# Performance work log

Hardware: AMD Instinct MI355X
Metric: run time of the kernel (lower is better)

## Reference

```python
import jax, jax.numpy as jnp
import numpy as np

B, L, D = 8, 2048, 1024


def _hippo(d, seed=0):
    # Author's 'hippo_matrix': Q @ diag(arctan(linspace(0, pi, d))) @ Q.T with Q orthogonal.
    rng = np.random.default_rng(seed)
    Q, _ = np.linalg.qr(rng.standard_normal((d, d)))
    Dm = np.diag(np.arctan(np.linspace(0.0, np.pi, d)))
    return (Q @ Dm @ Q.T).astype(np.float32)


def setup_inputs() -> dict:
    key = jax.random.key(0)
    k1, k2, k3, k4 = jax.random.split(key, 4)
    x = jax.random.normal(k1, (B, L, D), jnp.float32)
    A_w = jnp.asarray(_hippo(D))                                   # [D, D], spectral norm <= arctan(pi)
    C_w = jax.random.normal(k2, (D, D), jnp.float32) * (D ** -0.5)  # readout C
    # rc maps cat(x_t, y_{t-1}, y_container) (3D) -> D; small init keeps the
    # linear recurrence spectral radius < 1 so the 2048-step scan stays finite.
    rc_w = jax.random.normal(k3, (D, 3 * D), jnp.float32) * (0.2 / np.sqrt(3 * D))
    rc_b = jax.random.normal(k4, (D,), jnp.float32) * 0.02
    return {"x": x, "A_w": A_w, "C_w": C_w, "rc_w": rc_w, "rc_b": rc_b}


def reference(x, A_w, C_w, rc_w, rc_b):
    # y[0] = x[0]; y[t] = C @ A @ (rc_w @ cat(x[t], y[t-1], y[t-1]) + rc_b)
    # (prev output enters twice: once via the outer forward_step cat, once via
    #  the LinearRecurrentContainer's internal memory y).
    d = x.shape[-1]
    Wx = rc_w[:, :d]                          # acts on x_t
    Wy = rc_w[:, d:2 * d] + rc_w[:, 2 * d:]   # both copies of y_{t-1}
    M = C_w @ A_w                             # fused C∘A readout, [D, D]
    P = M @ Wx                                # input map
    Q = M @ Wy                                # recurrence map
    c = M @ rc_b                              # fused bias
    u = jnp.einsum('bld,ed->ble', x[:, 1:], P) + c  # driving terms for t >= 1, [B, L-1, D]
    y0 = x[:, 0]                              # parallel_scan copies the first input verbatim

    def step(y_prev, u_t):
        y = u_t + y_prev @ Q.T                # [B, D]
        return y, y

    _, ys = jax.lax.scan(step, y0, jnp.swapaxes(u, 0, 1))  # [L-1, B, D]
    return jnp.concatenate([y0[:, None, :], jnp.swapaxes(ys, 0, 1)], axis=1)  # [B, L, D]
```

## Files before the change

### kernel.cpp

```cpp
#include <hip/hip_runtime.h>

typedef unsigned short u16;
typedef unsigned int   u32;
typedef __attribute__((ext_vector_type(8))) short short8;
typedef __attribute__((ext_vector_type(4))) short short4v;
typedef __attribute__((ext_vector_type(4))) float f32x4;

struct SqJobs {
  const u16* a[4];
  const u16* b[4];
  u16* c[4];
  u16* ct[4];
};

__device__ __forceinline__ float bf2f(u16 v) {
  u32 x = ((u32)v) << 16;
  return __builtin_bit_cast(float, x);
}
__device__ __forceinline__ u16 f2bf(float f) {
  u32 x = __builtin_bit_cast(u32, f);
  x += 0x7FFFu + ((x >> 16) & 1u);
  return (u16)(x >> 16);
}
__device__ __forceinline__ void gload_lds16(const u16* g, u16* l) {
  __builtin_amdgcn_global_load_lds(
      (const __attribute__((address_space(1))) u32*)g,
      (__attribute__((address_space(3))) u32*)l, 16, 0, 0);
}

template <int BM, int BN, int ADT, int BDT, int EPI, int AMAP, int OMAP,
          int COUT, int TRW, int SQF>
__global__ __launch_bounds__(256) void gemm_nt(
    const void* __restrict__ Av, int lda, const void* __restrict__ Bv, int ldb,
    void* __restrict__ Cv, int ldc, int Mrows, int K,
    const float* __restrict__ zrowF, const u16* __restrict__ zrowB,
    const float* __restrict__ bias, const float* __restrict__ addf,
    float* __restrict__ Yout, u16* __restrict__ aux16, int jp1, int shoff,
    SqJobs jb) {
  constexpr int WM = BM / 2, WN = BN / 2;
  constexpr int MT = WM / 16, NTT = WN / 16;
  constexpr int AIn = ADT ? BM * 8 : BM * 4;
  constexpr int BIn = BDT ? BN * 8 : BN * 4;
  static_assert(AIn >= 256 && BIn >= 256, "tile too small for 256 threads");
  constexpr int AI = AIn / 256, BI = BIn / 256;
  constexpr int LA = BM * 32, LB = BN * 32;
  __shared__ u16 lA[2 * LA];
  __shared__ u16 lB[2 * LB];
  const int tid = threadIdx.x;
  const int lane = tid & 63, wid = tid >> 6;
  const int wm = wid & 1, wn = wid >> 1;
  const bool role = (SQF == 1) && ((int)blockIdx.x >= 32);
  const int pi = role ? (((int)blockIdx.x - 32) >> 4) : 0;
  const int bxe = role ? (((int)blockIdx.x - 32) & 15) : (int)blockIdx.x;
  const int m0 = bxe * BM, n0 = blockIdx.y * BN;
  const int effM = role ? 1024 : Mrows;
  const int q = lane >> 4, lm = lane & 15;
  const int cq = (q ^ (lm & 3)) * 8;

  const u16* corrB = nullptr;
  if constexpr (EPI == 7)
    corrB = (blockIdx.z == 0)
                ? (const u16*)Bv
                : jb.a[0] + (long)((int)blockIdx.z - 1) * 1048576;

  f32x4 acc[MT][NTT];
#pragma unroll
  for (int mi = 0; mi < MT; ++mi)
#pragma unroll
    for (int ni = 0; ni < NTT; ++ni) acc[mi][ni] = (f32x4){0.f, 0.f, 0.f, 0.f};

  const u16* aB[AI];
  const float* aF[AI];
#pragma unroll
  for (int i = 0; i < AI; ++i) {
    int g = tid + i * 256;
    int r = ADT ? (g >> 3) : (g >> 2);
    int c = ADT ? (g & 7) : (g & 3);
    int row = m0 + r;
    bool valid = (row < effM);
    if (AMAP == 1 && !role) {
      int p = row % 257;
      if (p < shoff) valid = false;
      row -= shoff;
    }
    if constexpr (ADT == 1) {
      int cs = ((((c >> 1) ^ (r & 3)) << 1) | (c & 1)) * 4;
      aF[i] = (valid ? (const float*)Av + (long)row * lda : zrowF) + cs;
    } else {
      int cs = (c ^ (r & 3)) * 8;
      const u16* base;
      if (role)
        base = jb.a[pi] + (long)row * 1024;
      else
        base = valid ? (const u16*)Av + (long)row * lda : zrowB;
      aB[i] = base + cs;
    }
  }
  const u16* bB[BI];
  const float* bF[BI];
#pragma unroll
  for (int i = 0; i < BI; ++i) {
    int g = tid + i * 256;
    int r = BDT ? (g >> 3) : (g >> 2);
    int c = BDT ? (g & 7) : (g & 3);
    if constexpr (BDT == 1) {
      int cs = ((((c >> 1) ^ (r & 3)) << 1) | (c & 1)) * 4;
      bF[i] = (const float*)Bv + (long)(n0 + r) * ldb + cs;
    } else {
      int cs = (c ^ (r & 3)) * 8;
      const u16* base;
      if (role) {
        base = jb.b[pi] + (long)(n0 + r) * 1024;
      } else {
        if constexpr (EPI == 7)
          base = corrB + (long)(n0 + r) * ldb;
        else
          base = (const u16*)Bv + (long)(n0 + r) * ldb;
      }
      bB[i] = base + cs;
    }
  }

  if constexpr (ADT == 1) {
    f32x4 f0[AI];
#pragma unroll
    for (int i = 0; i < AI; ++i) f0[i] = *(const f32x4*)(aF[i]);
#pragma unroll
    for (int i = 0; i < AI; ++i) {
      short4v s = {(short)f2bf(f0[i][0]), (short)f2bf(f0[i][1]),
                   (short)f2bf(f0[i][2]), (short)f2bf(f0[i][3])};
      *(short4v*)&lA[(tid + i * 256) * 4] = s;
    }
  } else {
#pragma unroll
    for (int i = 0; i < AI; ++i) gload_lds16(aB[i], &lA[(tid + i * 256) * 8]);
  }
  if constexpr (BDT == 1) {
    f32x4 f0[BI];
#pragma unroll
    for (int i = 0; i < BI; ++i) f0[i] = *(const f32x4*)(bF[i]);
#pragma unroll
    for (int i = 0; i < BI; ++i) {
      short4v s = {(short)f2bf(f0[i][0]), (short)f2bf(f0[i][1]),
                   (short)f2bf(f0[i][2]), (short)f2bf(f0[i][3])};
      *(short4v*)&lB[(tid + i * 256) * 4] = s;
    }
  } else {
#pragma unroll
    for (int i = 0; i < BI; ++i) gload_lds16(bB[i], &lB[(tid + i * 256) * 8]);
  }
  __syncthreads();

  int cur = 0;
  for (int k0 = 0; k0 < K; k0 += 32) {
    const int kn = k0 + 32;
    const bool more = kn < K;
    const int nxA = (cur ^ 1) * LA, nxB = (cur ^ 1) * LB;
    f32x4 fa[AI], fb[BI];
    if (more) {
      if constexpr (ADT == 1) {
#pragma unroll
        for (int i = 0; i < AI; ++i) fa[i] = *(const f32x4*)(aF[i] + kn);
      } else {
#pragma unroll
        for (int i = 0; i < AI; ++i)
          gload_lds16(aB[i] + kn, &lA[nxA + (tid + i * 256) * 8]);
      }
      if constexpr (BDT == 1) {
#pragma unroll
        for (int i = 0; i < BI; ++i) fb[i] = *(const f32x4*)(bF[i] + kn);
      } else {
#pragma unroll
        for (int i = 0; i < BI; ++i)
          gload_lds16(bB[i] + kn, &lB[nxB + (tid + i * 256) * 8]);
      }
    }
    short8 af[MT], bf[NTT];
#pragma unroll
    for (int mi = 0; mi < MT; ++mi)
      af[mi] =
          *(const short8*)&lA[cur * LA + (wm * WM + mi * 16 + lm) * 32 + cq];
#pragma unroll
    for (int ni = 0; ni < NTT; ++ni)
      bf[ni] =
          *(const short8*)&lB[cur * LB + (wn * WN + ni * 16 + lm) * 32 + cq];
#pragma unroll
    for (int mi = 0; mi < MT; ++mi)
#pragma unroll
      for (int ni = 0; ni < NTT; ++ni)
        acc[mi][ni] = __builtin_amdgcn_mfma_f32_16x16x32_bf16(
            af[mi], bf[ni], acc[mi][ni], 0, 0, 0);
    if (more) {
      if constexpr (ADT == 1) {
#pragma unroll
        for (int i = 0; i < AI; ++i) {
          short4v s = {(short)f2bf(fa[i][0]), (short)f2bf(fa[i][1]),
                       (short)f2bf(fa[i][2]), (short)f2bf(fa[i][3])};
          *(short4v*)&lA[nxA + (tid + i * 256) * 4] = s;
        }
      }
      if constexpr (BDT == 1) {
#pragma unroll
        for (int i = 0; i < BI; ++i) {
          short4v s = {(short)f2bf(fb[i][0]), (short)f2bf(fb[i][1]),
                       (short)f2bf(fb[i][2]), (short)f2bf(fb[i][3])};
          *(short4v*)&lB[nxB + (tid + i * 256) * 4] = s;
        }
      }
    }
    __syncthreads();
    cur ^= 1;
  }

#pragma unroll
  for (int mi = 0; mi < MT; ++mi) {
    int rbase = m0 + wm * WM + mi * 16 + q * 4;
#pragma unroll
    for (int ni = 0; ni < NTT; ++ni) {
      int ocol = n0 + wn * WN + ni * 16 + lm;
#pragma unroll
      for (int r = 0; r < 4; ++r) {
        int orow = rbase + r;
        float v = acc[mi][ni][r];
        if (role) {
          if (orow < 1024) {
            u16 ov = f2bf(v);
            jb.c[pi][(long)orow * 1024 + ocol] = ov;
            if (jb.ct[pi]) jb.ct[pi][(long)ocol * 1024 + orow] = ov;
          }
          continue;
        }
        if (orow >= Mrows) continue;
        if constexpr (EPI == 7) {
          long urow = 8L * orow + ((int)blockIdx.z + 1);
          float vv = v + addf[urow * 1024 + ocol];
          Yout[urow * 1024 + ocol] = vv;
          continue;
        }
        if constexpr (EPI == 5) {
          v += bias[ocol];
          bool isT0 = (orow & 2047) == 0;
          if (isT0) v = addf[(long)orow * 1024 + ocol];
          ((float*)Cv)[(long)orow * ldc + ocol] = v;
          if (isT0) Yout[((long)(orow >> 11) * 257) * 1024 + ocol] = v;
          if ((orow & 7) == 1)
            aux16[((long)(orow >> 3)) * 1024 + ocol] = f2bf(v);
          continue;
        }
        if constexpr (EPI == 6) {
          v += addf[(long)orow * 1024 + ocol];
          ((float*)Cv)[(long)orow * ldc + ocol] = v;
          int b = orow / 257;
          int pp_ = orow - b * 257;
          if (pp_ < 256)
            aux16[((long)(b * 256 + pp_)) * 1024 + ocol] = f2bf(v);
          if (pp_ >= 1 && pp_ < 256)
            Yout[((long)b * 2048 + 8L * pp_) * 1024 + ocol] = v;
          continue;
        }
        long urow = 0;
        bool uok = true;
        if constexpr (EPI == 2 || EPI == 3) {
          urow = 8L * orow + jp1;
          uok = ((urow & 2047) != 0);
          if (uok) v += addf[urow * 1024 + ocol];
        }
        if constexpr (EPI == 4) v += addf[(long)orow * 1024 + ocol];
        long wrow = orow;
        if constexpr (OMAP == 1)
          wrow = (long)(orow >> 8) * 257 + (orow & 255) + 1;
        if constexpr (COUT == 1)
          ((float*)Cv)[wrow * (long)ldc + ocol] = v;
        else
          ((u16*)Cv)[wrow * (long)ldc + ocol] = f2bf(v);
        if constexpr (TRW == 1) aux16[(long)ocol * ldc + orow] = f2bf(v);
        if constexpr (EPI == 3) {
          if (uok) Yout[urow * 1024 + ocol] = v;
        }
      }
    }
  }
}

__global__ void zero_misc(float* zF, u16* zB) {
  for (int i = threadIdx.x; i < 2048; i += 256) {
    zF[i] = 0.f;
    zB[i] = 0;
  }
}
__global__ void xconv(const float* __restrict__ x, u16* __restrict__ xb) {
  long i = (long)blockIdx.x * 256 + threadIdx.x;
  f32x4 v = ((const f32x4*)x)[i];
  short4v s = {(short)f2bf(v[0]), (short)f2bf(v[1]), (short)f2bf(v[2]),
               (short)f2bf(v[3])};
  ((short4v*)xb)[i] = s;
}
__global__ void prep_wt(const float* __restrict__ rc_w, u16* __restrict__ WxT,
                        u16* __restrict__ WyT) {
  __shared__ u16 tx[64][65];
  __shared__ u16 ty[64][65];
  int kb = blockIdx.x * 64, db = blockIdx.y * 64;
  for (int i = threadIdx.x; i < 64 * 64; i += 256) {
    int r = i >> 6, c = i & 63;
    long base = (long)(kb + r) * 3072 + db + c;
    tx[r][c] = f2bf(rc_w[base]);
    ty[r][c] = f2bf(rc_w[base + 1024] + rc_w[base + 2048]);
  }
  __syncthreads();
  for (int i = threadIdx.x; i < 64 * 64; i += 256) {
    int r = i >> 6, c = i & 63;
    WxT[(long)(db + r) * 1024 + kb + c] = tx[c][r];
    WyT[(long)(db + r) * 1024 + kb + c] = ty[c][r];
  }
}
__global__ void matvec_c(const u16* __restrict__ M_,
                         const float* __restrict__ rb,
                         float* __restrict__ cvec) {
  int row = blockIdx.x;
  int lane = threadIdx.x;
  float s = 0.f;
  for (int k = lane; k < 1024; k += 64)
    s += bf2f(M_[(long)row * 1024 + k]) * rb[k];
  for (int o = 32; o > 0; o >>= 1) s += __shfl_down(s, o, 64);
  if (lane == 0) cvec[row] = s;
}

extern "C" void kernel_launch(void* const* d_in, const int* in_sizes, int n_in,
                              void* d_out, int out_size, void* d_ws,
                              size_t ws_size, hipStream_t stream) {
  const float* x = (const float*)d_in[0];
  const float* A_w = (const float*)d_in[1];
  const float* C_w = (const float*)d_in[2];
  const float* rc_w = (const float*)d_in[3];
  const float* rc_b = (const float*)d_in[4];
  float* Y = (float*)d_out;

  char* ws = (char*)d_ws;
  const long MB = 1 << 20;
  u16* Z0 = (u16*)(ws);
  u16* Z1 = (u16*)(ws + 4 * MB);
  float* Bnd0 = (float*)(ws + 8 * MB);
  float* Bnd1 = (float*)(ws + 8 * MB + 8912896);
  char* p = ws + 25 * MB;
  u16* Mbuf = (u16*)p;
  u16* WxT = (u16*)(p + 2 * MB);
  u16* WyT = (u16*)(p + 4 * MB);
  u16* Pbuf = (u16*)(p + 6 * MB);
  u16* Qbuf = (u16*)(p + 8 * MB);
  u16* QbufT = (u16*)(p + 10 * MB);
  float* cvec = (float*)(p + 12 * MB);
  float* zF = (float*)(p + 12 * MB + 4096);
  u16* zB = (u16*)(p + 12 * MB + 12288);
  u16* xbf = (u16*)(p + 12 * MB + 16384);
  const size_t need_fast = (size_t)(25 * MB + 12 * MB + 16384) + 33554432;
  const bool fast = ws_size >= need_fast;

  SqJobs J0{};
  dim3 blk(256);
  zero_misc<<<dim3(1), blk, 0, stream>>>(zF, zB);
  if (fast) xconv<<<dim3(16384), blk, 0, stream>>>(x, xbf);
  prep_wt<<<dim3(16, 16), blk, 0, stream>>>(rc_w, WxT, WyT);

  gemm_nt<64, 64, 1, 1, 0, 0, 0, 0, 0, 0><<<dim3(16, 16), blk, 0, stream>>>(
      C_w, 1024, A_w, 1024, Mbuf, 1024, 1024, 1024, zF, zB, nullptr, nullptr,
      nullptr, nullptr, 0, 0, J0);
  gemm_nt<64, 64, 0, 0, 0, 0, 0, 0, 0, 0><<<dim3(16, 16), blk, 0, stream>>>(
      Mbuf, 1024, WxT, 1024, Pbuf, 1024, 1024, 1024, zF, zB, nullptr, nullptr,
      nullptr, nullptr, 0, 0, J0);
  gemm_nt<64, 64, 0, 0, 0, 0, 0, 0, 1, 0><<<dim3(16, 16), blk, 0, stream>>>(
      Mbuf, 1024, WyT, 1024, Qbuf, 1024, 1024, 1024, zF, zB, nullptr, nullptr,
      nullptr, QbufT, 0, 0, J0);
  matvec_c<<<dim3(1024), dim3(64), 0, stream>>>(Mbuf, rc_b, cvec);

  if (fast)
    gemm_nt<128, 128, 0, 0, 5, 0, 0, 1, 0, 0>
        <<<dim3(128, 8), blk, 0, stream>>>(xbf, 1024, Pbuf, 1024, Y, 1024,
                                           16384, 1024, zF, zB, cvec, x, Bnd0,
                                           Z0, 0, 0, J0);
  else
    gemm_nt<128, 128, 1, 0, 5, 0, 0, 1, 0, 0>
        <<<dim3(128, 8), blk, 0, stream>>>(x, 1024, Pbuf, 1024, Y, 1024, 16384,
                                           1024, zF, zB, cvec, x, Bnd0, Z0, 0,
                                           0, J0);

  if (fast) {
    const long M1 = 1048576;
    u16* PW = xbf;
    u16* Q2 = PW + 0 * M1;
    u16* Q3 = PW + 1 * M1;
    u16* Q4 = PW + 2 * M1;
    u16* Q5 = PW + 3 * M1;
    u16* Q6 = PW + 4 * M1;
    u16* Q7 = PW + 5 * M1;
    u16* Tb2 = xbf + 6 * M1;
    u16* Tt2 = xbf + 7 * M1;
    u16* Tb3 = xbf + 8 * M1;
    u16* Tt3 = xbf + 9 * M1;
    u16* Tb4 = xbf + 10 * M1;
    u16* Tt4 = xbf + 11 * M1;
    u16* Tb5 = xbf + 12 * M1;
    u16* Tt5 = xbf + 13 * M1;
    u16* Tb6 = xbf + 14 * M1;
    u16* Tt6 = xbf + 15 * M1;
    u16* Tt0 = Mbuf;
    u16* Tt1 = WxT;
    u16* Pw3T = WyT;

    SqJobs sj[7] = {};
    int nsq[7] = {1, 2, 4, 1, 1, 1, 1};
    sj[0].a[0] = Qbuf;  sj[0].b[0] = QbufT; sj[0].c[0] = Q2;  sj[0].ct[0] = Tt0;
    sj[1].a[0] = Q2;    sj[1].b[0] = Tt0;   sj[1].c[0] = Q4;  sj[1].ct[0] = Tt1;
    sj[1].a[1] = Q2;    sj[1].b[1] = QbufT; sj[1].c[1] = Q3;  sj[1].ct[1] = Pw3T;
    sj[2].a[0] = Q4;    sj[2].b[0] = Tt1;   sj[2].c[0] = Tb2; sj[2].ct[0] = Tt2;
    sj[2].a[1] = Q4;    sj[2].b[1] = QbufT; sj[2].c[1] = Q5;
    sj[2].a[2] = Q4;    sj[2].b[2] = Tt0;   sj[2].c[2] = Q6;
    sj[2].a[3] = Q4;    sj[2].b[3] = Pw3T;  sj[2].c[3] = Q7;
    sj[3].a[0] = Tb2;   sj[3].b[0] = Tt2;   sj[3].c[0] = Tb3; sj[3].ct[0] = Tt3;
    sj[4].a[0] = Tb3;   sj[4].b[0] = Tt3;   sj[4].c[0] = Tb4; sj[4].ct[0] = Tt4;
    sj[5].a[0] = Tb4;   sj[5].b[0] = Tt4;   sj[5].c[0] = Tb5; sj[5].ct[0] = Tt5;
    sj[6].a[0] = Tb5;   sj[6].b[0] = Tt5;   sj[6].c[0] = Tb6; sj[6].ct[0] = Tt6;

    for (int j = 1; j <= 6; ++j) {
      const u16* zin = (j & 1) ? Z0 : Z1;
      u16* zout = (j & 1) ? Z1 : Z0;
      gemm_nt<64, 64, 0, 0, 3, 0, 0, 0, 0, 1>
          <<<dim3(32 + 16 * nsq[j - 1], 16), blk, 0, stream>>>(
              zin, 1024, Qbuf, 1024, zout, 1024, 2048, 1024, zF, zB, nullptr,
              Y, Y, nullptr, j + 1, 0, sj[j - 1]);
    }
    gemm_nt<64, 64, 0, 0, 2, 0, 1, 1, 0, 1><<<dim3(48, 16), blk, 0, stream>>>(
        Z0, 1024, Qbuf, 1024, Bnd0, 1024, 2048, 1024, zF, zB, nullptr, Y,
        nullptr, nullptr, 8, 0, sj[6]);

    u16* TbP2[5] = {Tb2, Tb3, Tb4, Tb5, Tb6};
    float* bc = Bnd0;
    float* bn = Bnd1;
    for (int s = 0; s < 5; ++s) {
      if (s < 4)
        gemm_nt<64, 64, 1, 0, 4, 1, 0, 1, 0, 0>
            <<<dim3(33, 16), blk, 0, stream>>>(bc, 1024, TbP2[s], 1024, bn,
                                               1024, 2056, 1024, zF, zB,
                                               nullptr, bc, nullptr, nullptr,
                                               0, 1 << s, J0);
      else
        gemm_nt<64, 64, 1, 0, 6, 1, 0, 1, 0, 0>
            <<<dim3(33, 16), blk, 0, stream>>>(bc, 1024, TbP2[s], 1024, bn,
                                               1024, 2056, 1024, zF, zB,
                                               nullptr, bc, Y, Z0, 0, 1 << s,
                                               J0);
      float* t = bc;
      bc = bn;
      bn = t;
    }

    SqJobs cj{};
    cj.a[0] = PW;
    gemm_nt<64, 64, 0, 0, 7, 0, 0, 0, 0, 0>
        <<<dim3(32, 16, 7), blk, 0, stream>>>(Z0, 1024, Qbuf, 1024, Z1, 1024,
                                              2048, 1024, zF, zB, nullptr, Y,
                                              Y, nullptr, 0, 0, cj);
  } else {
    u16* Tb[7];
    u16* Tt[7];
    for (int i = 0; i < 7; ++i) {
      Tb[i] = (i & 1) ? Mbuf : WxT;
      Tt[i] = (i & 1) ? Pbuf : WyT;
    }
    for (int j = 1; j <= 6; ++j) {
      const u16* zin = (j & 1) ? Z0 : Z1;
      u16* zout = (j & 1) ? Z1 : Z0;
      gemm_nt<64, 64, 0, 0, 2, 0, 0, 0, 0, 0>
          <<<dim3(32, 16), blk, 0, stream>>>(zin, 1024, Qbuf, 1024, zout, 1024,
                                             2048, 1024, zF, zB, nullptr, Y,
                                             nullptr, nullptr, j + 1, 0, J0);
    }
    gemm_nt<64, 64, 0, 0, 2, 0, 1, 1, 0, 0><<<dim3(32, 16), blk, 0, stream>>>(
        Z0, 1024, Qbuf, 1024, Bnd0, 1024, 2048, 1024, zF, zB, nullptr, Y,
        nullptr, nullptr, 8, 0, J0);
    for (int i = 0; i < 3; ++i) {
      const u16* si = (i == 0) ? Qbuf : Tb[i - 1];
      const u16* st = (i == 0) ? QbufT : Tt[i - 1];
      gemm_nt<64, 64, 0, 0, 0, 0, 0, 0, 1, 0>
          <<<dim3(16, 16), blk, 0, stream>>>(si, 1024, st, 1024, Tb[i], 1024,
                                             1024, 1024, zF, zB, nullptr,
                                             nullptr, nullptr, Tt[i], 0, 0,
                                             J0);
    }
    float* bc = Bnd0;
    float* bn = Bnd1;
    for (int s = 0; s < 5; ++s) {
      if (s < 4)
        gemm_nt<64, 64, 1, 0, 4, 1, 0, 1, 0, 0>
            <<<dim3(33, 16), blk, 0, stream>>>(bc, 1024, Tb[s + 2], 1024, bn,
                                               1024, 2056, 1024, zF, zB,
                                               nullptr, bc, nullptr, nullptr,
                                               0, 1 << s, J0);
      else
        gemm_nt<64, 64, 1, 0, 6, 1, 0, 1, 0, 0>
            <<<dim3(33, 16), blk, 0, stream>>>(bc, 1024, Tb[s + 2], 1024, bn,
                                               1024, 2056, 1024, zF, zB,
                                               nullptr, bc, Y, Z0, 0, 1 << s,
                                               J0);
      if (s < 4) {
        int i = s + 3;
        gemm_nt<64, 64, 0, 0, 0, 0, 0, 0, 1, 0>
            <<<dim3(16, 16), blk, 0, stream>>>(Tb[i - 1], 1024, Tt[i - 1],
                                               1024, Tb[i], 1024, 1024, 1024,
                                               zF, zB, nullptr, nullptr,
                                               nullptr, Tt[i], 0, 0, J0);
      }
      float* t = bc;
      bc = bn;
      bn = t;
    }
    for (int j = 0; j <= 7; ++j) {
      const u16* zin = (j & 1) ? Z1 : Z0;
      u16* zout = (j & 1) ? Z0 : Z1;
      gemm_nt<64, 64, 0, 0, 3, 0, 0, 0, 0, 0>
          <<<dim3(32, 16), blk, 0, stream>>>(zin, 1024, Qbuf, 1024, zout, 1024,
                                             2048, 1024, zF, zB, nullptr, Y, Y,
                                             nullptr, j + 1, 0, J0);
    }
  }
}
```

Measured before the change: 649.9 us.

## Add triple-buffered async LDS pipeline for bf16 64x64 GEMMs and merge P/Q launches

For bf16-by-bf16 64x64 tiles, the GEMM main loop now uses three LDS buffers. Global-to-LDS loads are issued two k-steps ahead, with an explicit vmcnt wait and one barrier per step instead of the double-buffered two-sync scheme. The SQF template parameter becomes a block-offset threshold, so the P = M·Wx and Q = M·Wy GEMMs can share one launch with a side-job role, which removes a kernel launch. The extra LDS buffer raises shared memory per block, and the hand-placed waitcnt/barrier ordering relies on the exact count of outstanding loads.

New measurement: 649.1 us. No clear change (-0.1%).

```diff
diff --git a/kernel.cpp b/kernel.cpp
--- a/kernel.cpp
+++ b/kernel.cpp
@@ -44,14 +44,16 @@
   static_assert(AIn >= 256 && BIn >= 256, "tile too small for 256 threads");
   constexpr int AI = AIn / 256, BI = BIn / 256;
   constexpr int LA = BM * 32, LB = BN * 32;
-  __shared__ u16 lA[2 * LA];
-  __shared__ u16 lB[2 * LB];
+  constexpr bool PIPE3 = (ADT == 0 && BDT == 0 && BM == 64 && BN == 64);
+  constexpr int NBUF = PIPE3 ? 3 : 2;
+  __shared__ u16 lA[NBUF * LA];
+  __shared__ u16 lB[NBUF * LB];
   const int tid = threadIdx.x;
   const int lane = tid & 63, wid = tid >> 6;
   const int wm = wid & 1, wn = wid >> 1;
-  const bool role = (SQF == 1) && ((int)blockIdx.x >= 32);
-  const int pi = role ? (((int)blockIdx.x - 32) >> 4) : 0;
-  const int bxe = role ? (((int)blockIdx.x - 32) & 15) : (int)blockIdx.x;
+  const bool role = (SQF > 0) && ((int)blockIdx.x >= SQF);
+  const int pi = role ? (((int)blockIdx.x - SQF) >> 4) : 0;
+  const int bxe = role ? (((int)blockIdx.x - SQF) & 15) : (int)blockIdx.x;
   const int m0 = bxe * BM, n0 = blockIdx.y * BN;
   const int effM = role ? 1024 : Mrows;
   const int q = lane >> 4, lm = lane & 15;
@@ -121,95 +123,138 @@
     }
   }
 
-  if constexpr (ADT == 1) {
-    f32x4 f0[AI];
-#pragma unroll
-    for (int i = 0; i < AI; ++i) f0[i] = *(const f32x4*)(aF[i]);
-#pragma unroll
-    for (int i = 0; i < AI; ++i) {
-      short4v s = {(short)f2bf(f0[i][0]), (short)f2bf(f0[i][1]),
-                   (short)f2bf(f0[i][2]), (short)f2bf(f0[i][3])};
-      *(short4v*)&lA[(tid + i * 256) * 4] = s;
+  if constexpr (PIPE3) {
+    static_assert(AI == 1 && BI == 1, "PIPE3 assumes 1+1 issues/thread");
+    gload_lds16(aB[0], &lA[tid * 8]);
+    gload_lds16(bB[0], &lB[tid * 8]);
+    gload_lds16(aB[0] + 32, &lA[LA + tid * 8]);
+    gload_lds16(bB[0] + 32, &lB[LB + tid * 8]);
+    const int NS = K >> 5;
+    int cb = 0, pb = 2;
+    for (int ks = 0; ks < NS; ++ks) {
+      __builtin_amdgcn_sched_barrier(0);
+      if (ks + 1 < NS)
+        asm volatile("s_waitcnt vmcnt(2)" ::: "memory");
+      else
+        asm volatile("s_waitcnt vmcnt(0)" ::: "memory");
+      __builtin_amdgcn_s_barrier();
+      __builtin_amdgcn_sched_barrier(0);
+      if (ks + 2 < NS) {
+        const int kp = (ks + 2) << 5;
+        gload_lds16(aB[0] + kp, &lA[pb * LA + tid * 8]);
+        gload_lds16(bB[0] + kp, &lB[pb * LB + tid * 8]);
+      }
+      const int ca = cb * LA, cbb = cb * LB;
+      short8 af[MT], bfr[NTT];
+#pragma unroll
+      for (int mi = 0; mi < MT; ++mi)
+        af[mi] = *(const short8*)&lA[ca + (wm * WM + mi * 16 + lm) * 32 + cq];
+#pragma unroll
+      for (int ni = 0; ni < NTT; ++ni)
+        bfr[ni] =
+            *(const short8*)&lB[cbb + (wn * WN + ni * 16 + lm) * 32 + cq];
+#pragma unroll
+      for (int mi = 0; mi < MT; ++mi)
+#pragma unroll
+        for (int ni = 0; ni < NTT; ++ni)
+          acc[mi][ni] = __builtin_amdgcn_mfma_f32_16x16x32_bf16(
+              af[mi], bfr[ni], acc[mi][ni], 0, 0, 0);
+      cb = (cb == 2) ? 0 : cb + 1;
+      pb = (pb == 2) ? 0 : pb + 1;
     }
   } else {
-#pragma unroll
-    for (int i = 0; i < AI; ++i) gload_lds16(aB[i], &lA[(tid + i * 256) * 8]);
-  }
-  if constexpr (BDT == 1) {
-    f32x4 f0[BI];
-#pragma unroll
-    for (int i = 0; i < BI; ++i) f0[i] = *(const f32x4*)(bF[i]);
-#pragma unroll
-    for (int i = 0; i < BI; ++i) {
-      short4v s = {(short)f2bf(f0[i][0]), (short)f2bf(f0[i][1]),
-                   (short)f2bf(f0[i][2]), (short)f2bf(f0[i][3])};
-      *(short4v*)&lB[(tid + i * 256) * 4] = s;
-    }
-  } else {
-#pragma unroll
-    for (int i = 0; i < BI; ++i) gload_lds16(bB[i], &lB[(tid + i * 256) * 8]);
-  }
-  __syncthreads();
-
-  int cur = 0;
-  for (int k0 = 0; k0 < K; k0 += 32) {
-    const int kn = k0 + 32;
-    const bool more = kn < K;
-    const int nxA = (cur ^ 1) * LA, nxB = (cur ^ 1) * LB;
-    f32x4 fa[AI], fb[BI];
-    if (more) {
-      if constexpr (ADT == 1) {
-#pragma unroll
-        for (int i = 0; i < AI; ++i) fa[i] = *(const f32x4*)(aF[i] + kn);
-      } else {
-#pragma unroll
-        for (int i = 0; i < AI; ++i)
-          gload_lds16(aB[i] + kn, &lA[nxA + (tid + i * 256) * 8]);
-      }
-      if constexpr (BDT == 1) {
-#pragma unroll
-        for (int i = 0; i < BI; ++i) fb[i] = *(const f32x4*)(bF[i] + kn);
-      } else {
-#pragma unroll
-        for (int i = 0; i < BI; ++i)
-          gload_lds16(bB[i] + kn, &lB[nxB + (tid + i * 256) * 8]);
-      }
-    }
-    short8 af[MT], bf[NTT];
-#pragma unroll
-    for (int mi = 0; mi < MT; ++mi)
-      af[mi] =
-          *(const short8*)&lA[cur * LA + (wm * WM + mi * 16 + lm) * 32 + cq];
-#pragma unroll
-    for (int ni = 0; ni < NTT; ++ni)
-      bf[ni] =
-          *(const short8*)&lB[cur * LB + (wn * WN + ni * 16 + lm) * 32 + cq];
-#pragma unroll
-    for (int mi = 0; mi < MT; ++mi)
+    if constexpr (ADT == 1) {
+      f32x4 f0[AI];
+#pragma unroll
+      for (int i = 0; i < AI; ++i) f0[i] = *(const f32x4*)(aF[i]);
+#pragma unroll
+      for (int i = 0; i < AI; ++i) {
+        short4v s = {(short)f2bf(f0[i][0]), (short)f2bf(f0[i][1]),
+                     (short)f2bf(f0[i][2]), (short)f2bf(f0[i][3])};
+        *(short4v*)&lA[(tid + i * 256) * 4] = s;
+      }
+    } else {
+#pragma unroll
+      for (int i = 0; i < AI; ++i)
+        gload_lds16(aB[i], &lA[(tid + i * 256) * 8]);
+    }
+    if constexpr (BDT == 1) {
+      f32x4 f0[BI];
+#pragma unroll
+      for (int i = 0; i < BI; ++i) f0[i] = *(const f32x4*)(bF[i]);
+#pragma unroll
+      for (int i = 0; i < BI; ++i) {
+        short4v s = {(short)f2bf(f0[i][0]), (short)f2bf(f0[i][1]),
+                     (short)f2bf(f0[i][2]), (short)f2bf(f0[i][3])};
+        *(short4v*)&lB[(tid + i * 256) * 4] = s;
+      }
+    } else {
+#pragma unroll
+      for (int i = 0; i < BI; ++i)
+        gload_lds16(bB[i], &lB[(tid + i * 256) * 8]);
+    }
+    __syncthreads();
+
+    int cur = 0;
+    for (int k0 = 0; k0 < K; k0 += 32) {
+      const int kn = k0 + 32;
+      const bool more = kn < K;
+      const int nxA = (cur ^ 1) * LA, nxB = (cur ^ 1) * LB;
+      f32x4 fa[AI], fb[BI];
+      if (more) {
+        if constexpr (ADT == 1) {
+#pragma unroll
+          for (int i = 0; i < AI; ++i) fa[i] = *(const f32x4*)(aF[i] + kn);
+        } else {
+#pragma unroll
+          for (int i = 0; i < AI; ++i)
+            gload_lds16(aB[i] + kn, &lA[nxA + (tid + i * 256) * 8]);
+        }
+        if constexpr (BDT == 1) {
+#pragma unroll
+          for (int i = 0; i < BI; ++i) fb[i] = *(const f32x4*)(bF[i] + kn);
+        } else {
+#pragma unroll
+          for (int i = 0; i < BI; ++i)
+            gload_lds16(bB[i] + kn, &lB[nxB + (tid + i * 256) * 8]);
+        }
+      }
+      short8 af[MT], bf[NTT];
+#pragma unroll
+      for (int mi = 0; mi < MT; ++mi)
+        af[mi] =
+            *(const short8*)&lA[cur * LA + (wm * WM + mi * 16 + lm) * 32 + cq];
 #pragma unroll
       for (int ni = 0; ni < NTT; ++ni)
-        acc[mi][ni] = __builtin_amdgcn_mfma_f32_16x16x32_bf16(
-            af[mi], bf[ni], acc[mi][ni], 0, 0, 0);
-    if (more) {
-      if constexpr (ADT == 1) {
-#pragma unroll
-        for (int i = 0; i < AI; ++i) {
-          short4v s = {(short)f2bf(fa[i][0]), (short)f2bf(fa[i][1]),
-                       (short)f2bf(fa[i][2]), (short)f2bf(fa[i][3])};
-          *(short4v*)&lA[nxA + (tid + i * 256) * 4] = s;
-        }
-      }
-      if constexpr (BDT == 1) {
-#pragma unroll
-        for (int i = 0; i < BI; ++i) {
-          short4v s = {(short)f2bf(fb[i][0]), (short)f2bf(fb[i][1]),
-                       (short)f2bf(fb[i][2]), (short)f2bf(fb[i][3])};
-          *(short4v*)&lB[nxB + (tid + i * 256) * 4] = s;
-        }
-      }
-    }
-    __syncthreads();
-    cur ^= 1;
+        bf[ni] =
+            *(const short8*)&lB[cur * LB + (wn * WN + ni * 16 + lm) * 32 + cq];
+#pragma unroll
+      for (int mi = 0; mi < MT; ++mi)
+#pragma unroll
+        for (int ni = 0; ni < NTT; ++ni)
+          acc[mi][ni] = __builtin_amdgcn_mfma_f32_16x16x32_bf16(
+              af[mi], bf[ni], acc[mi][ni], 0, 0, 0);
+      if (more) {
+        if constexpr (ADT == 1) {
+#pragma unroll
+          for (int i = 0; i < AI; ++i) {
+            short4v s = {(short)f2bf(fa[i][0]), (short)f2bf(fa[i][1]),
+                         (short)f2bf(fa[i][2]), (short)f2bf(fa[i][3])};
+            *(short4v*)&lA[nxA + (tid + i * 256) * 4] = s;
+          }
+        }
+        if constexpr (BDT == 1) {
+#pragma unroll
+          for (int i = 0; i < BI; ++i) {
+            short4v s = {(short)f2bf(fb[i][0]), (short)f2bf(fb[i][1]),
+                         (short)f2bf(fb[i][2]), (short)f2bf(fb[i][3])};
+            *(short4v*)&lB[nxB + (tid + i * 256) * 4] = s;
+          }
+        }
+      }
+      __syncthreads();
+      cur ^= 1;
+    }
   }
 
 #pragma unroll
@@ -364,12 +409,13 @@
   gemm_nt<64, 64, 1, 1, 0, 0, 0, 0, 0, 0><<<dim3(16, 16), blk, 0, stream>>>(
       C_w, 1024, A_w, 1024, Mbuf, 1024, 1024, 1024, zF, zB, nullptr, nullptr,
       nullptr, nullptr, 0, 0, J0);
-  gemm_nt<64, 64, 0, 0, 0, 0, 0, 0, 0, 0><<<dim3(16, 16), blk, 0, stream>>>(
-      Mbuf, 1024, WxT, 1024, Pbuf, 1024, 1024, 1024, zF, zB, nullptr, nullptr,
-      nullptr, nullptr, 0, 0, J0);
-  gemm_nt<64, 64, 0, 0, 0, 0, 0, 0, 1, 0><<<dim3(16, 16), blk, 0, stream>>>(
+  SqJobs sjPQ{};
+  sjPQ.a[0] = Mbuf;
+  sjPQ.b[0] = WxT;
+  sjPQ.c[0] = Pbuf;
+  gemm_nt<64, 64, 0, 0, 0, 0, 0, 0, 1, 16><<<dim3(32, 16), blk, 0, stream>>>(
       Mbuf, 1024, WyT, 1024, Qbuf, 1024, 1024, 1024, zF, zB, nullptr, nullptr,
-      nullptr, QbufT, 0, 0, J0);
+      nullptr, QbufT, 0, 0, sjPQ);
   matvec_c<<<dim3(1024), dim3(64), 0, stream>>>(Mbuf, rc_b, cvec);
 
   if (fast)
@@ -386,12 +432,6 @@
   if (fast) {
     const long M1 = 1048576;
     u16* PW = xbf;
-    u16* Q2 = PW + 0 * M1;
-    u16* Q3 = PW + 1 * M1;
-    u16* Q4 = PW + 2 * M1;
-    u16* Q5 = PW + 3 * M1;
-    u16* Q6 = PW + 4 * M1;
-    u16* Q7 = PW + 5 * M1;
     u16* Tb2 = xbf + 6 * M1;
     u16* Tt2 = xbf + 7 * M1;
     u16* Tb3 = xbf + 8 * M1;
@@ -408,27 +448,27 @@
 
     SqJobs sj[7] = {};
     int nsq[7] = {1, 2, 4, 1, 1, 1, 1};
-    sj[0].a[0] = Qbuf;  sj[0].b[0] = QbufT; sj[0].c[0] = Q2;  sj[0].ct[0] = Tt0;
-    sj[1].a[0] = Q2;    sj[1].b[0] = Tt0;   sj[1].c[0] = Q4;  sj[1].ct[0] = Tt1;
-    sj[1].a[1] = Q2;    sj[1].b[1] = QbufT; sj[1].c[1] = Q3;  sj[1].ct[1] = Pw3T;
-    sj[2].a[0] = Q4;    sj[2].b[0] = Tt1;   sj[2].c[0] = Tb2; sj[2].ct[0] = Tt2;
-    sj[2].a[1] = Q4;    sj[2].b[1] = QbufT; sj[2].c[1] = Q5;
-    sj[2].a[2] = Q4;    sj[2].b[2] = Tt0;   sj[2].c[2] = Q6;
-    sj[2].a[3] = Q4;    sj[2].b[3] = Pw3T;  sj[2].c[3] = Q7;
-    sj[3].a[0] = Tb2;   sj[3].b[0] = Tt2;   sj[3].c[0] = Tb3; sj[3].ct[0] = Tt3;
-    sj[4].a[0] = Tb3;   sj[4].b[0] = Tt3;   sj[4].c[0] = Tb4; sj[4].ct[0] = Tt4;
-    sj[5].a[0] = Tb4;   sj[5].b[0] = Tt4;   sj[5].c[0] = Tb5; sj[5].ct[0] = Tt5;
-    sj[6].a[0] = Tb5;   sj[6].b[0] = Tt5;   sj[6].c[0] = Tb6; sj[6].ct[0] = Tt6;
+    sj[0].a[0] = Qbuf;        sj[0].b[0] = QbufT; sj[0].c[0] = PW;          sj[0].ct[0] = Tt0;
+    sj[1].a[0] = PW;          sj[1].b[0] = Tt0;   sj[1].c[0] = PW + 2 * M1; sj[1].ct[0] = Tt1;
+    sj[1].a[1] = PW;          sj[1].b[1] = QbufT; sj[1].c[1] = PW + 1 * M1; sj[1].ct[1] = Pw3T;
+    sj[2].a[0] = PW + 2 * M1; sj[2].b[0] = Tt1;   sj[2].c[0] = Tb2;         sj[2].ct[0] = Tt2;
+    sj[2].a[1] = PW + 2 * M1; sj[2].b[1] = QbufT; sj[2].c[1] = PW + 3 * M1;
+    sj[2].a[2] = PW + 2 * M1; sj[2].b[2] = Tt0;   sj[2].c[2] = PW + 4 * M1;
+    sj[2].a[3] = PW + 2 * M1; sj[2].b[3] = Pw3T;  sj[2].c[3] = PW + 5 * M1;
+    sj[3].a[0] = Tb2;         sj[3].b[0] = Tt2;   sj[3].c[0] = Tb3;         sj[3].ct[0] = Tt3;
+    sj[4].a[0] = Tb3;         sj[4].b[0] = Tt3;   sj[4].c[0] = Tb4;         sj[4].ct[0] = Tt4;
+    sj[5].a[0] = Tb4;         sj[5].b[0] = Tt4;   sj[5].c[0] = Tb5;         sj[5].ct[0] = Tt5;
+    sj[6].a[0] = Tb5;         sj[6].b[0] = Tt5;   sj[6].c[0] = Tb6;         sj[6].ct[0] = Tt6;
 
     for (int j = 1; j <= 6; ++j) {
       const u16* zin = (j & 1) ? Z0 : Z1;
       u16* zout = (j & 1) ? Z1 : Z0;
-      gemm_nt<64, 64, 0, 0, 3, 0, 0, 0, 0, 1>
+      gemm_nt<64, 64, 0, 0, 3, 0, 0, 0, 0, 32>
           <<<dim3(32 + 16 * nsq[j - 1], 16), blk, 0, stream>>>(
               zin, 1024, Qbuf, 1024, zout, 1024, 2048, 1024, zF, zB, nullptr,
               Y, Y, nullptr, j + 1, 0, sj[j - 1]);
     }
-    gemm_nt<64, 64, 0, 0, 2, 0, 1, 1, 0, 1><<<dim3(48, 16), blk, 0, stream>>>(
+    gemm_nt<64, 64, 0, 0, 2, 0, 1, 1, 0, 32><<<dim3(48, 16), blk, 0, stream>>>(
         Z0, 1024, Qbuf, 1024, Bnd0, 1024, 2048, 1024, zF, zB, nullptr, Y,
         nullptr, nullptr, 8, 0, sj[6]);
 
```
